# Optimization experiments

Hardware: AMD Instinct MI355X
Metric: run time of the kernel (lower is better)

Reference implementation:

```python
import jax, jax.numpy as jnp
import numpy as np
from itertools import product

L_LEVELS = 3
PAD = 2
DN = ('NCH', 'OIH', 'NCH')


def _realign(S, L):
    # Faithful port of SCI_Net.realign(): order of concatenated leaves, then inverse perm.
    out = []
    for comb in product((0, 1), repeat=L):
        v = np.arange(S)
        for b in comb:
            v = v[b::2] if b == 1 else v[::2]
        out.append(v)
    order = np.concatenate(out)          # concat position -> original time index
    return np.argsort(order)             # original-time-sorted positions (row1 of `a`)


def _conv_op(x, w1, w2):
    # ReplicationPad1d -> Conv1d(C->C*e) -> LeakyReLU(0.01) -> Dropout(eval=id) -> Conv1d(C*e->C) -> Tanh
    xp = jnp.pad(x, ((0, 0), (0, 0), (PAD, PAD)), mode='edge')
    h = jax.lax.conv_general_dilated(xp, w1, (1,), 'VALID', dimension_numbers=DN)
    h = jnp.where(h > 0, h, 0.01 * h)
    h = jax.lax.conv_general_dilated(h, w2, (1,), 'VALID', dimension_numbers=DN)
    return jnp.tanh(h)


def setup_inputs() -> dict:
    key = jax.random.key(0)
    ks = jax.random.split(key, 7)
    B, C, S, E, K = 128, 8, 8192, 4, 3
    return {
        'x': jax.random.normal(ks[0], (B, C, S), jnp.float32),
        'conv_w1': jax.random.normal(ks[1], (L_LEVELS, 4, C * E, C, K), jnp.float32) * 0.2,
        'conv_w2': jax.random.normal(ks[2], (L_LEVELS, 4, C, C * E, K), jnp.float32) * 0.1,
        'fc1_w': jax.random.normal(ks[3], (50, S), jnp.float32) * 0.01,
        'fc1_b': jax.random.normal(ks[4], (50,), jnp.float32) * 0.01,
        'fc2_w': jax.random.normal(ks[5], (24, 50), jnp.float32) * 0.1,
        'fc2_b': jax.random.normal(ks[6], (24,), jnp.float32) * 0.01,
    }


def reference(x, conv_w1, conv_w2, fc1_w, fc1_b, fc2_w, fc2_b):
    B, C, S = x.shape
    prev = x[None]  # [n_branch=1, B, C, T]
    for lvl in range(L_LEVELS):
        n, _, _, T = prev.shape
        xb = prev.reshape(n * B, C, T)
        # NOTE: idx_even = arange(1,T,2), idx_odd = arange(0,T,2) in the source.
        F_even = xb[:, :, 1::2]
        F_odd = xb[:, :, 0::2]
        w1, w2 = conv_w1[lvl], conv_w2[lvl]  # op order: 0=nu, 1=psi, 2=ro, 3=phi (shared across branches)
        F_even_s = F_even * jnp.exp(_conv_op(F_odd, w1[1], w2[1]))   # psi
        F_odd_s = F_odd * jnp.exp(_conv_op(F_even, w1[3], w2[3]))    # phi
        F_even_final = F_odd_s - _conv_op(F_odd_s, w1[0], w2[0])     # nu
        F_odd_final = F_even_s + _conv_op(F_even_s, w1[2], w2[2])    # ro
        T2 = T // 2
        new = jnp.stack([F_even_final.reshape(n, B, C, T2),
                         F_odd_final.reshape(n, B, C, T2)], axis=1)  # [n, 2, B, C, T2]
        prev = new.reshape(2 * n, B, C, T2)
    ridx = jnp.asarray(_realign(S, L_LEVELS))
    F_concat = jnp.transpose(prev, (1, 2, 0, 3)).reshape(B, C, S)  # concat leaves on time dim
    F_concat = F_concat[:, :, ridx] + x                            # reverse-index scatter + residual
    h = jax.nn.relu(jnp.einsum('bcs,hs->bch', F_concat, fc1_w) + fc1_b)
    return jnp.einsum('bch,oh->bco', h, fc2_w) + fc2_b  # [B, C, horizon]
```

## Files before the change

### kernel.cpp

```cpp
#include <hip/hip_runtime.h>

#define TT   128
#define TIN2 (TT + 8)
#define NHA  (TT + 6)
#define NEO  (TT + 4)
#define NHB  (TT + 2)
#define HROW 44

typedef _Float16 h2 __attribute__((ext_vector_type(2)));
typedef __fp16 fp16v2 __attribute__((ext_vector_type(2)));
typedef _Float16 f16x4 __attribute__((ext_vector_type(4)));
typedef _Float16 f16x8 __attribute__((ext_vector_type(8)));
typedef float f32x4 __attribute__((ext_vector_type(4)));

__device__ _Float16 g_w1A[12][2][64][8];
__device__ _Float16 g_w2A[12][3][64][8];

__device__ __forceinline__ h2 pkh(float a, float b) {
  fp16v2 r = __builtin_amdgcn_cvt_pkrtz(a, b);
  return __builtin_bit_cast(h2, r);
}
__device__ __forceinline__ unsigned int pku(float a, float b) {
  return __builtin_bit_cast(unsigned int, pkh(a, b));
}
__device__ __forceinline__ float fast_tanh(float x) {
  return 1.f - __fdividef(2.f, __expf(2.f * x) + 1.f);
}
__device__ __forceinline__ unsigned int lky(unsigned int u) {
  h2 v = __builtin_bit_cast(h2, u);
  h2 s = v * (h2){(_Float16)0.01f, (_Float16)0.01f};
  h2 m = __builtin_elementwise_max(v, s);
  return __builtin_bit_cast(unsigned int, m);
}
__device__ __forceinline__ float lane_spread(float a_low, float b_low, int lane) {
  float s = __shfl_xor(b_low, 32);
  return (lane >= 32) ? s : a_low;
}
__device__ __forceinline__ f16x8 ld_hid(const _Float16* p) {
  const f16x4 lo = *(const f16x4*)p;
  const f16x4 hi = *(const f16x4*)(p + 4);
  f16x8 r;
  r[0] = lo[0]; r[1] = lo[1]; r[2] = lo[2]; r[3] = lo[3];
  r[4] = hi[0]; r[5] = hi[1]; r[6] = hi[2]; r[7] = hi[3];
  return r;
}

__global__ __launch_bounds__(256) void pack_mfma(
    const float* __restrict__ w1, const float* __restrict__ w2)
{
  int id = blockIdx.x * 256 + threadIdx.x;
  if (id >= 12 * 5 * 64) return;
  const int lane = id & 63;
  const int rest = id >> 6;
  const int slot = rest % 5;
  const int pr   = rest / 5;
  if (slot < 2) {
    const int oc = slot * 16 + (lane & 15);
    const int bb = lane >> 4;
#pragma unroll
    for (int j = 0; j < 8; ++j) {
      float v = (bb < 3) ? w1[((size_t)pr * 32 + oc) * 24 + j * 3 + bb] : 0.f;
      g_w1A[pr][slot][lane][j] = (_Float16)v;
    }
  } else {
    const int t = slot - 2;
    const int oc = lane & 15;
#pragma unroll
    for (int j = 0; j < 8; ++j) {
      const int hc = 8 * (lane >> 4) + j;
      float v = (oc < 8) ? w2[((size_t)pr * 8 + oc) * 96 + hc * 3 + t] : 0.f;
      g_w2A[pr][t][lane][j] = (_Float16)v;
    }
  }
}

template <bool IN16>
__global__ __launch_bounds__(256) void level_fused(
    const void* __restrict__ Xv, _Float16* __restrict__ NEXT,
    int lvl, int T2, int tilesPerSeq)
{
  __shared__ _Float16 inS[2][TIN2][8];
  __shared__ _Float16 hidS[2][NHA][HROW];
  __shared__ _Float16 esS[2][NEO][8];

  const int blk = blockIdx.x;
  const int nb  = blk / tilesPerSeq;
  const int t0  = (blk - nb * tilesPerSeq) * TT;

  if constexpr (IN16) {
    const _Float16* Xh = (const _Float16*)Xv;
    const unsigned int* Xu = (const unsigned int*)(Xh + (size_t)nb * 8 * (2 * (size_t)T2));
    for (int jj = threadIdx.x; jj < TIN2; jj += 256) {
      int j = t0 - 4 + jj;
      j = j < 0 ? 0 : (j > T2 - 1 ? T2 - 1 : j);
      unsigned int u0[4], u1[4];
#pragma unroll
      for (int cp = 0; cp < 4; ++cp) {
        const h2 va = __builtin_bit_cast(h2, Xu[(size_t)(2 * cp) * T2 + j]);
        const h2 vb = __builtin_bit_cast(h2, Xu[(size_t)(2 * cp + 1) * T2 + j]);
        u0[cp] = __builtin_bit_cast(unsigned int, (h2){va[0], vb[0]});
        u1[cp] = __builtin_bit_cast(unsigned int, (h2){va[1], vb[1]});
      }
      *(uint4*)&inS[0][jj][0] = make_uint4(u0[0], u0[1], u0[2], u0[3]);
      *(uint4*)&inS[1][jj][0] = make_uint4(u1[0], u1[1], u1[2], u1[3]);
    }
  } else {
    const float* X = (const float*)Xv;
    const float2* Xrow = (const float2*)(X + (size_t)nb * 8 * (2 * (size_t)T2));
    for (int jj = threadIdx.x; jj < TIN2; jj += 256) {
      int j = t0 - 4 + jj;
      j = j < 0 ? 0 : (j > T2 - 1 ? T2 - 1 : j);
      unsigned int u0[4], u1[4];
#pragma unroll
      for (int cp = 0; cp < 4; ++cp) {
        float2 a = Xrow[(size_t)(2 * cp) * T2 + j];
        float2 b = Xrow[(size_t)(2 * cp + 1) * T2 + j];
        u0[cp] = pku(a.x, b.x);
        u1[cp] = pku(a.y, b.y);
      }
      *(uint4*)&inS[0][jj][0] = make_uint4(u0[0], u0[1], u0[2], u0[3]);
      *(uint4*)&inS[1][jj][0] = make_uint4(u1[0], u1[1], u1[2], u1[3]);
    }
  }
  __syncthreads();

  const int wid  = __builtin_amdgcn_readfirstlane((int)(threadIdx.x >> 6));
  const int lane = threadIdx.x & 63;
  const int side = wid >> 1, half = wid & 1;
  const int g = lane >> 4, col = lane & 15;
  const int tb = half * 64;
  const int rp = ((lane >> 4) & 1) * 2 + (lane >> 5);

  const int pa = lvl * 4 + (side ? 3 : 1);
  const int pb = lvl * 4 + (side ? 2 : 0);
  const f16x8 a1w0 = *(const f16x8*)&g_w1A[pa][0][lane][0];
  const f16x8 a1w1 = *(const f16x8*)&g_w1A[pa][1][lane][0];
  const f16x8 a2w0 = *(const f16x8*)&g_w2A[pa][0][lane][0];
  const f16x8 a2w1 = *(const f16x8*)&g_w2A[pa][1][lane][0];
  const f16x8 a2w2 = *(const f16x8*)&g_w2A[pa][2][lane][0];
  const f16x8 b1w0 = *(const f16x8*)&g_w1A[pb][0][lane][0];
  const f16x8 b1w1 = *(const f16x8*)&g_w1A[pb][1][lane][0];
  const f16x8 b2w0 = *(const f16x8*)&g_w2A[pb][0][lane][0];
  const f16x8 b2w1 = *(const f16x8*)&g_w2A[pb][1][lane][0];
  const f16x8 b2w2 = *(const f16x8*)&g_w2A[pb][2][lane][0];
  const f32x4 zero = {0.f, 0.f, 0.f, 0.f};

#pragma unroll
  for (int nt = 0; nt < 5; ++nt) {
    const int row = tb + nt * 16 + col;
    const int rr = (row + g > TIN2 - 1) ? (TIN2 - 1) : (row + g);
    const f16x8 bf = *(const f16x8*)&inS[side][rr][0];
    f32x4 d0 = __builtin_amdgcn_mfma_f32_16x16x32_f16(a1w0, bf, zero, 0, 0, 0);
    f32x4 d1 = __builtin_amdgcn_mfma_f32_16x16x32_f16(a1w1, bf, zero, 0, 0, 0);
    if (row < NHA) {
      *(uint2*)&hidS[side][row][4 * g] =
          make_uint2(lky(pku(d0[0], d0[1])), lky(pku(d0[2], d0[3])));
      *(uint2*)&hidS[side][row][16 + 4 * g] =
          make_uint2(lky(pku(d1[0], d1[1])), lky(pku(d1[2], d1[3])));
    }
  }
  __syncthreads();

#pragma unroll
  for (int nt = 0; nt < 5; ++nt) {
    const int row = tb + nt * 16 + col;
    f32x4 acc = zero;
    {
      int rr = (row     > NHA - 1) ? (NHA - 1) : row;
      acc = __builtin_amdgcn_mfma_f32_16x16x32_f16(a2w0, ld_hid(&hidS[side][rr][8 * g]), acc, 0, 0, 0);
      rr = (row + 1 > NHA - 1) ? (NHA - 1) : (row + 1);
      acc = __builtin_amdgcn_mfma_f32_16x16x32_f16(a2w1, ld_hid(&hidS[side][rr][8 * g]), acc, 0, 0, 0);
      rr = (row + 2 > NHA - 1) ? (NHA - 1) : (row + 2);
      acc = __builtin_amdgcn_mfma_f32_16x16x32_f16(a2w2, ld_hid(&hidS[side][rr][8 * g]), acc, 0, 0, 0);
    }
    if (row < NEO) {
      const float va = lane_spread(acc[0], acc[2], lane);
      const float vb = lane_spread(acc[1], acc[3], lane);
      const h2 mpk = *(const h2*)&inS[side ^ 1][row + 2][2 * rp];
      const float v0 = (float)mpk[0] * __expf(fast_tanh(va));
      const float v1 = (float)mpk[1] * __expf(fast_tanh(vb));
      *(unsigned int*)&esS[side][row][2 * rp] = pku(v0, v1);
    }
  }
  __syncthreads();

  const int srcB = side ^ 1;
  const int eoLo = (t0 == 0) ? 2 : 0;
  const int eoHi = (t0 + TT >= T2) ? (TT + 1) : (NEO - 1);
#pragma unroll
  for (int nt = 0; nt < 5; ++nt) {
    const int row = tb + nt * 16 + col;
    int rr = row + g;
    rr = rr < eoLo ? eoLo : (rr > eoHi ? eoHi : rr);
    const f16x8 bf = *(const f16x8*)&esS[srcB][rr][0];
    f32x4 d0 = __builtin_amdgcn_mfma_f32_16x16x32_f16(b1w0, bf, zero, 0, 0, 0);
    f32x4 d1 = __builtin_amdgcn_mfma_f32_16x16x32_f16(b1w1, bf, zero, 0, 0, 0);
    if (row < NHB) {
      *(uint2*)&hidS[side][row][4 * g] =
          make_uint2(lky(pku(d0[0], d0[1])), lky(pku(d0[2], d0[3])));
      *(uint2*)&hidS[side][row][16 + 4 * g] =
          make_uint2(lky(pku(d1[0], d1[1])), lky(pku(d1[2], d1[3])));
    }
  }
  __syncthreads();

  const float sgn = side ? 1.f : -1.f;
  const int i = nb >> 7;
  const int b = nb & 127;
  const int outseq = 2 * i + side;
#pragma unroll
  for (int nt = 0; nt < 4; ++nt) {
    const int row = half * 64 + nt * 16 + col;
    f32x4 acc = zero;
    acc = __builtin_amdgcn_mfma_f32_16x16x32_f16(b2w0, ld_hid(&hidS[side][row][8 * g]), acc, 0, 0, 0);
    acc = __builtin_amdgcn_mfma_f32_16x16x32_f16(b2w1, ld_hid(&hidS[side][row + 1][8 * g]), acc, 0, 0, 0);
    acc = __builtin_amdgcn_mfma_f32_16x16x32_f16(b2w2, ld_hid(&hidS[side][row + 2][8 * g]), acc, 0, 0, 0);
    const float va = lane_spread(acc[0], acc[2], lane);
    const float vb = lane_spread(acc[1], acc[3], lane);
    const h2 base = *(const h2*)&esS[srcB][row + 2][2 * rp];
    const int tg = t0 + row;
    const int c0 = 2 * rp;
    NEXT[(((size_t)outseq * 128 + b) * 8 + c0) * T2 + tg]     = (_Float16)((float)base[0] + sgn * fast_tanh(va));
    NEXT[(((size_t)outseq * 128 + b) * 8 + c0 + 1) * T2 + tg] = (_Float16)((float)base[1] + sgn * fast_tanh(vb));
  }
}

__global__ __launch_bounds__(256) void fc1_fused(
    const _Float16* __restrict__ P, const float* __restrict__ x,
    const float* __restrict__ W, float* __restrict__ partial)
{
  const int rt = blockIdx.x & 31;
  const int ch = blockIdx.x >> 5;
  const int s0 = ch * 512;
  __shared__ unsigned int Fl[32][68];
  __shared__ unsigned int Wl[64][68];
  const int hg = threadIdx.x & 15;
  const int rg = threadIdx.x >> 4;
  float acc[2][4] = {{0.f, 0.f, 0.f, 0.f}, {0.f, 0.f, 0.f, 0.f}};

  for (int sb = 0; sb < 512; sb += 128) {
    __syncthreads();
    for (int i = threadIdx.x; i < 32 * 32; i += 256) {
      const int r = i >> 5, s4 = i & 31;
      const int row = rt * 32 + r;
      const int b = row >> 3, c = row & 7;
      const int base = s0 + sb + 4 * s4;
      const int t = base >> 3, r0 = base & 7;
      const float4 xv = *(const float4*)(x + (size_t)row * 8192 + base);
      _Float16 p[4];
#pragma unroll
      for (int j = 0; j < 4; ++j) {
        const int rr = r0 + j;
        const int rev = ((rr & 1) << 2) | (rr & 2) | ((rr >> 2) & 1);
        p[j] = P[(((size_t)rev * 128 + b) * 8 + c) * 1024 + t];
      }
      const h2 f01 = pkh(xv.x, xv.y) + (h2){p[0], p[1]};
      const h2 f23 = pkh(xv.z, xv.w) + (h2){p[2], p[3]};
      *(uint2*)&Fl[r][s4 * 2] = make_uint2(__builtin_bit_cast(unsigned int, f01),
                                           __builtin_bit_cast(unsigned int, f23));
    }
    for (int i = threadIdx.x; i < 64 * 32; i += 256) {
      const int hh = i >> 5, s4 = i & 31;
      float4 v = make_float4(0.f, 0.f, 0.f, 0.f);
      if (hh < 50) v = ((const float4*)(W + (size_t)hh * 8192 + s0 + sb))[s4];
      *(uint2*)&Wl[hh][s4 * 2] = make_uint2(pku(v.x, v.y), pku(v.z, v.w));
    }
    __syncthreads();
    for (int q = 0; q < 16; ++q) {
      const uint4 fa = *(const uint4*)&Fl[rg * 2][q * 4];
      const uint4 fb = *(const uint4*)&Fl[rg * 2 + 1][q * 4];
#pragma unroll
      for (int j = 0; j < 4; ++j) {
        const uint4 w = *(const uint4*)&Wl[hg + 16 * j][q * 4];
#pragma unroll
        for (int e = 0; e < 4; ++e) {
          const h2 we = __builtin_bit_cast(h2, (&w.x)[e]);
          acc[0][j] = __builtin_amdgcn_fdot2(we, __builtin_bit_cast(h2, (&fa.x)[e]), acc[0][j], false);
          acc[1][j] = __builtin_amdgcn_fdot2(we, __builtin_bit_cast(h2, (&fb.x)[e]), acc[1][j], false);
        }
      }
    }
  }
#pragma unroll
  for (int rr = 0; rr < 2; ++rr)
#pragma unroll
    for (int j = 0; j < 4; ++j)
      partial[((size_t)ch * 1024 + rt * 32 + rg * 2 + rr) * 64 + hg + 16 * j] = acc[rr][j];
}

__global__ __launch_bounds__(64) void fc_stage2(
    const float* __restrict__ partial, const float* __restrict__ fc1b,
    const float* __restrict__ fc2w, const float* __restrict__ fc2b,
    float* __restrict__ out)
{
  const int row = blockIdx.x;
  const int h = threadIdx.x;
  __shared__ float hs[64];
  float v = 0.f;
  if (h < 50) {
    for (int ch = 0; ch < 16; ++ch)
      v += partial[((size_t)ch * 1024 + row) * 64 + h];
    v += fc1b[h];
    v = v > 0.f ? v : 0.f;
  }
  hs[h] = v;
  __syncthreads();
  if (h < 24) {
    float a = fc2b[h];
    for (int j = 0; j < 50; ++j)
      a = fmaf(hs[j], fc2w[h * 50 + j], a);
    out[(size_t)row * 24 + h] = a;
  }
}

extern "C" void kernel_launch(void* const* d_in, const int* in_sizes, int n_in,
                              void* d_out, int out_size, void* d_ws, size_t ws_size,
                              hipStream_t stream)
{
  const float* x    = (const float*)d_in[0];
  const float* w1a  = (const float*)d_in[1];
  const float* w2a  = (const float*)d_in[2];
  const float* fc1w = (const float*)d_in[3];
  const float* fc1b = (const float*)d_in[4];
  const float* fc2w = (const float*)d_in[5];
  const float* fc2b = (const float*)d_in[6];
  float* out = (float*)d_out;

  _Float16* bufA = (_Float16*)d_ws;
  _Float16* bufB = bufA + (size_t)9 * 1024 * 1024;
  float* partial = (float*)((char*)d_ws + (size_t)40 * 1024 * 1024);

  pack_mfma<<<dim3(15), dim3(256), 0, stream>>>(w1a, w2a);

  level_fused<false><<<dim3(4096), dim3(256), 0, stream>>>(x,    bufA, 0, 4096, 32);
  level_fused<true ><<<dim3(4096), dim3(256), 0, stream>>>(bufA, bufB, 1, 2048, 16);
  level_fused<true ><<<dim3(4096), dim3(256), 0, stream>>>(bufB, bufA, 2, 1024, 8);

  fc1_fused<<<dim3(512), dim3(256), 0, stream>>>(bufA, x, fc1w, partial);
  fc_stage2<<<dim3(1024), dim3(64), 0, stream>>>(partial, fc1b, fc2w, fc2b, out);
  (void)in_sizes; (void)n_in; (void)out_size; (void)ws_size;
}
```

Baseline: 129.6 us.

## Store intermediate level buffers time-major with channels innermost; batch fc_stage2 rows

Changes the fp16 intermediate layout between levels from channel-major [seq][c][t] to time-major [seq][t][c]. Each thread now writes its two adjacent channels with one packed 32-bit store, and the next level loads a full 8-channel uint4 per timestep instead of eight strided loads plus shuffles. The fc1 gather is updated to the new layout, though its per-channel reads are now strided by 8 elements. Separately, fc_stage2 processes four rows per 256-thread block to cut the block count.

```diff
diff --git a/kernel.cpp b/kernel.cpp
--- a/kernel.cpp
+++ b/kernel.cpp
@@ -88,21 +88,12 @@
   const int t0  = (blk - nb * tilesPerSeq) * TT;
 
   if constexpr (IN16) {
-    const _Float16* Xh = (const _Float16*)Xv;
-    const unsigned int* Xu = (const unsigned int*)(Xh + (size_t)nb * 8 * (2 * (size_t)T2));
-    for (int jj = threadIdx.x; jj < TIN2; jj += 256) {
-      int j = t0 - 4 + jj;
-      j = j < 0 ? 0 : (j > T2 - 1 ? T2 - 1 : j);
-      unsigned int u0[4], u1[4];
-#pragma unroll
-      for (int cp = 0; cp < 4; ++cp) {
-        const h2 va = __builtin_bit_cast(h2, Xu[(size_t)(2 * cp) * T2 + j]);
-        const h2 vb = __builtin_bit_cast(h2, Xu[(size_t)(2 * cp + 1) * T2 + j]);
-        u0[cp] = __builtin_bit_cast(unsigned int, (h2){va[0], vb[0]});
-        u1[cp] = __builtin_bit_cast(unsigned int, (h2){va[1], vb[1]});
-      }
-      *(uint4*)&inS[0][jj][0] = make_uint4(u0[0], u0[1], u0[2], u0[3]);
-      *(uint4*)&inS[1][jj][0] = make_uint4(u1[0], u1[1], u1[2], u1[3]);
+    const _Float16* Xh = (const _Float16*)Xv + (size_t)nb * (2 * (size_t)T2) * 8;
+    for (int it = threadIdx.x; it < 2 * TIN2; it += 256) {
+      const int s = it & 1, jj = it >> 1;
+      int p = t0 - 4 + jj;
+      p = p < 0 ? 0 : (p > T2 - 1 ? T2 - 1 : p);
+      *(uint4*)&inS[s][jj][0] = *(const uint4*)&Xh[(size_t)(2 * p + s) * 8];
     }
   } else {
     const float* X = (const float*)Xv;
@@ -208,6 +199,7 @@
   const int i = nb >> 7;
   const int b = nb & 127;
   const int outseq = 2 * i + side;
+  _Float16* outbase = NEXT + ((size_t)outseq * 128 + b) * (size_t)T2 * 8;
 #pragma unroll
   for (int nt = 0; nt < 4; ++nt) {
     const int row = half * 64 + nt * 16 + col;
@@ -219,9 +211,8 @@
     const float vb = lane_spread(acc[1], acc[3], lane);
     const h2 base = *(const h2*)&esS[srcB][row + 2][2 * rp];
     const int tg = t0 + row;
-    const int c0 = 2 * rp;
-    NEXT[(((size_t)outseq * 128 + b) * 8 + c0) * T2 + tg]     = (_Float16)((float)base[0] + sgn * fast_tanh(va));
-    NEXT[(((size_t)outseq * 128 + b) * 8 + c0 + 1) * T2 + tg] = (_Float16)((float)base[1] + sgn * fast_tanh(vb));
+    *(unsigned int*)&outbase[(size_t)tg * 8 + 2 * rp] =
+        pku((float)base[0] + sgn * fast_tanh(va), (float)base[1] + sgn * fast_tanh(vb));
   }
 }
 
@@ -252,7 +243,7 @@
       for (int j = 0; j < 4; ++j) {
         const int rr = r0 + j;
         const int rev = ((rr & 1) << 2) | (rr & 2) | ((rr >> 2) & 1);
-        p[j] = P[(((size_t)rev * 128 + b) * 8 + c) * 1024 + t];
+        p[j] = P[(((size_t)rev * 128 + b) * 1024 + t) * 8 + c];
       }
       const h2 f01 = pkh(xv.x, xv.y) + (h2){p[0], p[1]};
       const h2 f23 = pkh(xv.z, xv.w) + (h2){p[2], p[3]};
@@ -288,14 +279,15 @@
       partial[((size_t)ch * 1024 + rt * 32 + rg * 2 + rr) * 64 + hg + 16 * j] = acc[rr][j];
 }
 
-__global__ __launch_bounds__(64) void fc_stage2(
+__global__ __launch_bounds__(256) void fc_stage2(
     const float* __restrict__ partial, const float* __restrict__ fc1b,
     const float* __restrict__ fc2w, const float* __restrict__ fc2b,
     float* __restrict__ out)
 {
-  const int row = blockIdx.x;
-  const int h = threadIdx.x;
-  __shared__ float hs[64];
+  const int rr = threadIdx.x >> 6;
+  const int row = blockIdx.x * 4 + rr;
+  const int h = threadIdx.x & 63;
+  __shared__ float hs[4][64];
   float v = 0.f;
   if (h < 50) {
     for (int ch = 0; ch < 16; ++ch)
@@ -303,12 +295,12 @@
     v += fc1b[h];
     v = v > 0.f ? v : 0.f;
   }
-  hs[h] = v;
+  hs[rr][h] = v;
   __syncthreads();
   if (h < 24) {
     float a = fc2b[h];
     for (int j = 0; j < 50; ++j)
-      a = fmaf(hs[j], fc2w[h * 50 + j], a);
+      a = fmaf(hs[rr][j], fc2w[h * 50 + j], a);
     out[(size_t)row * 24 + h] = a;
   }
 }
@@ -337,6 +329,6 @@
   level_fused<true ><<<dim3(4096), dim3(256), 0, stream>>>(bufB, bufA, 2, 1024, 8);
 
   fc1_fused<<<dim3(512), dim3(256), 0, stream>>>(bufA, x, fc1w, partial);
-  fc_stage2<<<dim3(1024), dim3(64), 0, stream>>>(partial, fc1b, fc2w, fc2b, out);
+  fc_stage2<<<dim3(256), dim3(256), 0, stream>>>(partial, fc1b, fc2w, fc2b, out);
   (void)in_sizes; (void)n_in; (void)out_size; (void)ws_size;
 }
```

Measured after the change: 128.3 us. About the same (-1.0%).
